# Performance work log

Hardware: AMD Instinct MI355X
Metric: run time of the kernel (lower is better)

Reference implementation:

```python
import jax, jax.numpy as jnp
import numpy as np

M, K, N = 4096, 7168, 18432  # tokens, in_features, out_features


def setup_inputs() -> dict:
    key = jax.random.key(0)
    kx, kw, ks = jax.random.split(key, 3)
    x = jax.random.normal(kx, (M, K), dtype=jnp.float32)
    # int8 quantized weight, layout [in_features, out_features] as in the torch module
    weight = jax.random.randint(kw, (K, N), -128, 128, dtype=jnp.int8)
    # per-output-channel dequant scale (bf16 in the original; fp32 here for a stable baseline)
    scale = jax.random.uniform(ks, (N,), dtype=jnp.float32) * 0.02 + 1e-3
    return {"x": x, "weight": weight, "scale": scale}


def reference(x, weight, scale):
    # Fused dequant + GEMM: y = x @ (int8_weight * scale_per_out_channel)
    w = weight.astype(x.dtype) * scale.astype(x.dtype)[None, :]  # [K, N]
    return x @ w  # [M, N]
```

## Files before the change

kernel.cpp:

```cpp
#include <hip/hip_runtime.h>
#include <hip/hip_bf16.h>
#include <cstdint>
#include <cstddef>

#define M_ 4096
#define K_ 7168
#define N_ 18432

typedef __attribute__((ext_vector_type(4))) int i32x4;

#define AS1 __attribute__((address_space(1)))
#define AS3 __attribute__((address_space(3)))

__device__ __forceinline__ void gld_lds16(void* lds, const void* g) {
  __builtin_amdgcn_global_load_lds((const AS1 void*)g, (AS3 void*)lds, 16, 0, 0);
}

__global__ __launch_bounds__(256) void quant_x_kernel(const float* __restrict__ x,
                                                      signed char* __restrict__ xq,
                                                      float* __restrict__ sx) {
  const int m = blockIdx.x;
  const float4* row4 = (const float4*)(x + (size_t)m * K_);
  float mx = 0.f;
  for (int i = threadIdx.x; i < K_ / 4; i += 256) {
    float4 v = row4[i];
    mx = fmaxf(mx, fmaxf(fmaxf(fabsf(v.x), fabsf(v.y)), fmaxf(fabsf(v.z), fabsf(v.w))));
  }
#pragma unroll
  for (int d = 1; d < 64; d <<= 1) mx = fmaxf(mx, __shfl_xor(mx, d));
  __shared__ float wred[4];
  if ((threadIdx.x & 63) == 0) wred[threadIdx.x >> 6] = mx;
  __syncthreads();
  mx = fmaxf(fmaxf(wred[0], wred[1]), fmaxf(wred[2], wred[3]));
  const float inv = mx > 0.f ? 127.f / mx : 0.f;
  if (threadIdx.x == 0) sx[m] = mx / 127.f;
  char4* q4 = (char4*)(xq + (size_t)m * K_);
  for (int i = threadIdx.x; i < K_ / 4; i += 256) {
    float4 v = row4[i];
    char4 c;
    c.x = (signed char)__float2int_rn(v.x * inv);
    c.y = (signed char)__float2int_rn(v.y * inv);
    c.z = (signed char)__float2int_rn(v.z * inv);
    c.w = (signed char)__float2int_rn(v.w * inv);
    q4[i] = c;
  }
}

__global__ __launch_bounds__(256) void transpose_w_kernel(const int* __restrict__ W,
                                                          signed char* __restrict__ Wt) {
  __shared__ __align__(16) signed char t[64][80];
  const int k0 = blockIdx.x * 64;
  const int n0 = blockIdx.y * 64;
  const int r = threadIdx.x >> 4;
  const int c4 = (threadIdx.x & 15) * 4;
#pragma unroll
  for (int rr = 0; rr < 4; ++rr) {
    const int row = rr * 16 + r;
    int4 v = *(const int4*)(W + (size_t)(k0 + row) * N_ + n0 + c4);
    t[c4 + 0][row] = (signed char)v.x;
    t[c4 + 1][row] = (signed char)v.y;
    t[c4 + 2][row] = (signed char)v.z;
    t[c4 + 3][row] = (signed char)v.w;
  }
  __syncthreads();
  const int nr = threadIdx.x >> 2;
  const int cb = (threadIdx.x & 3) * 16;
  int4 o = *(const int4*)&t[nr][cb];
  *(int4*)(Wt + (size_t)(n0 + nr) * K_ + k0 + cb) = o;
}

__global__ __launch_bounds__(256) void gemm_i8_kernel(const signed char* __restrict__ Aq,
                                                      const signed char* __restrict__ Bt,
                                                      const float* __restrict__ sx,
                                                      const float* __restrict__ scale,
                                                      float* __restrict__ C) {
  __shared__ __align__(16) signed char As[8192];
  __shared__ __align__(16) signed char Bs[8192];

  const int NBN = N_ / 128;
  const int per = (M_ / 128) * NBN / 8;
  const int bid = blockIdx.x;
  const int swz = (bid & 7) * per + (bid >> 3);
  const int bm = swz / NBN;
  const int bn = swz % NBN;
  const int m0 = bm * 128;
  const int n0 = bn * 128;

  const int tid = threadIdx.x;
  const int wid = tid >> 6;
  const int lane = tid & 63;
  const int wrow = wid >> 1;
  const int wcol = wid & 1;

  const int sr = tid >> 2;
  const int sc = (tid & 3) << 4;
  const signed char* a_src0 = Aq + (size_t)(m0 + sr) * K_ + sc;
  const signed char* a_src1 = a_src0 + (size_t)64 * K_;
  const signed char* b_src0 = Bt + (size_t)(n0 + sr) * K_ + sc;
  const signed char* b_src1 = b_src0 + (size_t)64 * K_;
  signed char* a_dst0 = As + wid * 1024;
  signed char* a_dst1 = As + 4096 + wid * 1024;
  signed char* b_dst0 = Bs + wid * 1024;
  signed char* b_dst1 = Bs + 4096 + wid * 1024;

  const int fr = lane & 15;
  const int ko = lane >> 4;
  const int a_off = (wrow * 64 + fr) * 64 + ko * 16;
  const int b_off = (wcol * 64 + fr) * 64 + ko * 16;

  i32x4 acc[4][4] = {};

  for (int k = 0; k < K_; k += 64) {
    gld_lds16(a_dst0, a_src0 + k);
    gld_lds16(a_dst1, a_src1 + k);
    gld_lds16(b_dst0, b_src0 + k);
    gld_lds16(b_dst1, b_src1 + k);
    __syncthreads();

    i32x4 av[4], bv[4];
#pragma unroll
    for (int i = 0; i < 4; ++i) av[i] = *(const i32x4*)(As + a_off + i * 1024);
#pragma unroll
    for (int j = 0; j < 4; ++j) bv[j] = *(const i32x4*)(Bs + b_off + j * 1024);
#pragma unroll
    for (int i = 0; i < 4; ++i)
#pragma unroll
      for (int j = 0; j < 4; ++j)
        acc[i][j] = __builtin_amdgcn_mfma_i32_16x16x64_i8(av[i], bv[j], acc[i][j], 0, 0, 0);
    __syncthreads();
  }

  const int mb = m0 + wrow * 64;
  const int nb = n0 + wcol * 64;
  const int col = lane & 15;
  const int rq = (lane >> 4) * 4;
  float scl[4];
#pragma unroll
  for (int j = 0; j < 4; ++j) scl[j] = scale[nb + j * 16 + col];
#pragma unroll
  for (int i = 0; i < 4; ++i) {
#pragma unroll
    for (int r = 0; r < 4; ++r) {
      const int m = mb + i * 16 + rq + r;
      const float s = sx[m];
      float* out = C + (size_t)m * N_ + nb + col;
#pragma unroll
      for (int j = 0; j < 4; ++j) out[j * 16] = (float)acc[i][j][r] * s * scl[j];
    }
  }
}

__global__ __launch_bounds__(256) void fb_gemm_kernel(const float* __restrict__ X,
                                                      const int* __restrict__ W,
                                                      const float* __restrict__ scale,
                                                      float* __restrict__ Y) {
  __shared__ float xs[16][65];
  __shared__ float ws_[16][65];
  const int bn = blockIdx.x * 64;
  const int bm = blockIdx.y * 64;
  const int tx = threadIdx.x & 15;
  const int ty = threadIdx.x >> 4;
  float acc[4][4] = {};
  for (int k0 = 0; k0 < K_; k0 += 16) {
    for (int i = threadIdx.x; i < 64 * 16; i += 256) {
      int r = i >> 4, c = i & 15;
      xs[c][r] = X[(size_t)(bm + r) * K_ + k0 + c];
    }
    for (int i = threadIdx.x; i < 16 * 64; i += 256) {
      int r = i >> 6, c = i & 63;
      ws_[r][c] = (float)W[(size_t)(k0 + r) * N_ + bn + c];
    }
    __syncthreads();
#pragma unroll
    for (int kk = 0; kk < 16; ++kk) {
      float a[4], b[4];
#pragma unroll
      for (int i = 0; i < 4; ++i) a[i] = xs[kk][ty * 4 + i];
#pragma unroll
      for (int j = 0; j < 4; ++j) b[j] = ws_[kk][tx * 4 + j];
#pragma unroll
      for (int i = 0; i < 4; ++i)
#pragma unroll
        for (int j = 0; j < 4; ++j) acc[i][j] += a[i] * b[j];
    }
    __syncthreads();
  }
#pragma unroll
  for (int i = 0; i < 4; ++i)
#pragma unroll
    for (int j = 0; j < 4; ++j)
      Y[(size_t)(bm + ty * 4 + i) * N_ + bn + tx * 4 + j] = acc[i][j] * scale[bn + tx * 4 + j];
}

extern "C" void kernel_launch(void* const* d_in, const int* in_sizes, int n_in,
                              void* d_out, int out_size, void* d_ws, size_t ws_size,
                              hipStream_t stream) {
  const float* x = (const float*)d_in[0];
  const int* w = (const int*)d_in[1];
  const float* scale = (const float*)d_in[2];
  float* y = (float*)d_out;

  const size_t xq_bytes = (size_t)M_ * K_;
  const size_t sx_off = xq_bytes;
  const size_t wt_off = sx_off + (size_t)M_ * 4;
  const size_t need = wt_off + (size_t)N_ * K_;

  if (ws_size >= need) {
    signed char* xq = (signed char*)d_ws;
    float* sx = (float*)((char*)d_ws + sx_off);
    signed char* wt = (signed char*)((char*)d_ws + wt_off);
    hipLaunchKernelGGL(quant_x_kernel, dim3(M_), dim3(256), 0, stream, x, xq, sx);
    hipLaunchKernelGGL(transpose_w_kernel, dim3(K_ / 64, N_ / 64), dim3(256), 0, stream, w, wt);
    hipLaunchKernelGGL(gemm_i8_kernel, dim3((M_ / 128) * (N_ / 128)), dim3(256), 0, stream,
                       xq, wt, sx, scale, y);
  } else {
    hipLaunchKernelGGL(fb_gemm_kernel, dim3(N_ / 64, M_ / 64), dim3(256), 0, stream,
                       x, w, scale, y);
  }
}
```

Before: 896.6 us.

## Rewrite int8 GEMM with 256x256 tiles, double-buffered LDS and swizzled loads

Replaces the 128x128, single-buffered int8 MFMA GEMM with a 256x256 tile run by 512 threads. Each step covers K=128 split into two 64-wide halves, and global-to-LDS prefetch is double-buffered and interleaved with MFMA phases using explicit waitcnt, barriers and setprio. An XOR swizzle on the LDS layout is meant to avoid bank conflicts. The aim is to hide global load latency and raise arithmetic intensity, at the cost of 128KB of LDS per block, heavy register use, and a fragile hand-tuned schedule.

```diff
diff --git a/kernel.cpp b/kernel.cpp
--- a/kernel.cpp
+++ b/kernel.cpp
@@ -6,6 +6,8 @@
 #define M_ 4096
 #define K_ 7168
 #define N_ 18432
+#define NT 56
+#define ITERS 28
 
 typedef __attribute__((ext_vector_type(4))) int i32x4;
 
@@ -69,85 +71,153 @@
   *(int4*)(Wt + (size_t)(n0 + nr) * K_ + k0 + cb) = o;
 }
 
-__global__ __launch_bounds__(256) void gemm_i8_kernel(const signed char* __restrict__ Aq,
-                                                      const signed char* __restrict__ Bt,
-                                                      const float* __restrict__ sx,
-                                                      const float* __restrict__ scale,
-                                                      float* __restrict__ C) {
-  __shared__ __align__(16) signed char As[8192];
-  __shared__ __align__(16) signed char Bs[8192];
-
-  const int NBN = N_ / 128;
-  const int per = (M_ / 128) * NBN / 8;
+__global__ __launch_bounds__(512, 2) void gemm_i8_kernel(const signed char* __restrict__ Aq,
+                                                         const signed char* __restrict__ Bt,
+                                                         const float* __restrict__ sx,
+                                                         const float* __restrict__ scale,
+                                                         float* __restrict__ C) {
+  __shared__ __align__(16) signed char lds[131072];
+
+  const int NBN = 72;
+  const int per = 144;
   const int bid = blockIdx.x;
   const int swz = (bid & 7) * per + (bid >> 3);
-  const int bm = swz / NBN;
-  const int bn = swz % NBN;
-  const int m0 = bm * 128;
-  const int n0 = bn * 128;
+  const int m0 = (swz / NBN) * 256;
+  const int n0 = (swz % NBN) * 256;
 
   const int tid = threadIdx.x;
-  const int wid = tid >> 6;
+  const int w = tid >> 6;
   const int lane = tid & 63;
-  const int wrow = wid >> 1;
-  const int wcol = wid & 1;
-
-  const int sr = tid >> 2;
-  const int sc = (tid & 3) << 4;
-  const signed char* a_src0 = Aq + (size_t)(m0 + sr) * K_ + sc;
-  const signed char* a_src1 = a_src0 + (size_t)64 * K_;
-  const signed char* b_src0 = Bt + (size_t)(n0 + sr) * K_ + sc;
-  const signed char* b_src1 = b_src0 + (size_t)64 * K_;
-  signed char* a_dst0 = As + wid * 1024;
-  signed char* a_dst1 = As + 4096 + wid * 1024;
-  signed char* b_dst0 = Bs + wid * 1024;
-  signed char* b_dst1 = Bs + 4096 + wid * 1024;
+  const int wr = w >> 2;
+  const int wc = w & 3;
 
   const int fr = lane & 15;
-  const int ko = lane >> 4;
-  const int a_off = (wrow * 64 + fr) * 64 + ko * 16;
-  const int b_off = (wcol * 64 + fr) * 64 + ko * 16;
-
-  i32x4 acc[4][4] = {};
-
-  for (int k = 0; k < K_; k += 64) {
-    gld_lds16(a_dst0, a_src0 + k);
-    gld_lds16(a_dst1, a_src1 + k);
-    gld_lds16(b_dst0, b_src0 + k);
-    gld_lds16(b_dst1, b_src1 + k);
-    __syncthreads();
-
-    i32x4 av[4], bv[4];
-#pragma unroll
-    for (int i = 0; i < 4; ++i) av[i] = *(const i32x4*)(As + a_off + i * 1024);
-#pragma unroll
-    for (int j = 0; j < 4; ++j) bv[j] = *(const i32x4*)(Bs + b_off + j * 1024);
-#pragma unroll
-    for (int i = 0; i < 4; ++i)
-#pragma unroll
-      for (int j = 0; j < 4; ++j)
-        acc[i][j] = __builtin_amdgcn_mfma_i32_16x16x64_i8(av[i], bv[j], acc[i][j], 0, 0, 0);
-    __syncthreads();
-  }
-
-  const int mb = m0 + wrow * 64;
-  const int nb = n0 + wcol * 64;
+  const int q = lane >> 4;
+  const int sl = ((q ^ ((fr >> 1) & 3)) << 4);
+
+  const int ls16 = (((lane & 3) ^ ((lane >> 3) & 3)) << 4);
+  const int pr0 = w * 16 + (lane >> 2);
+  const unsigned offA0 = (unsigned)(m0 + pr0) * K_ + ls16;
+  const unsigned offA1 = (unsigned)(m0 + 128 + pr0) * K_ + ls16;
+  const unsigned offB0 = (unsigned)(n0 + pr0) * K_ + ls16;
+  const unsigned offB1 = (unsigned)(n0 + 128 + pr0) * K_ + ls16;
+
+#define STAGE_A(T, KS) do {                                                        \
+    const int tc_ = (T) < NT ? (T) : NT - 1;                                       \
+    signed char* d_ = lds + (((T) & 1) * 32768 + (KS) * 16384 + w * 1024);         \
+    gld_lds16(d_, Aq + (size_t)offA0 + tc_ * 128 + (KS) * 64);                     \
+    gld_lds16(d_ + 8192, Aq + (size_t)offA1 + tc_ * 128 + (KS) * 64);              \
+  } while (0)
+#define STAGE_B(T, KS) do {                                                        \
+    const int tc_ = (T) < NT ? (T) : NT - 1;                                       \
+    signed char* d_ = lds + (65536 + ((T) & 1) * 32768 + (KS) * 16384 + w * 1024); \
+    gld_lds16(d_, Bt + (size_t)offB0 + tc_ * 128 + (KS) * 64);                     \
+    gld_lds16(d_ + 8192, Bt + (size_t)offB1 + tc_ * 128 + (KS) * 64);              \
+  } while (0)
+#define LDA(BUF, KS, MH) do {                                                      \
+    const signed char* ab = lds + ((BUF) * 32768 + (KS) * 16384);                  \
+    _Pragma("unroll") for (int i_ = 0; i_ < 4; ++i_)                               \
+      aq[i_] = *(const i32x4*)(ab + (wr * 128 + ((MH) * 4 + i_) * 16 + fr) * 64 + sl); \
+  } while (0)
+#define LDB(BUF, KS) do {                                                          \
+    const signed char* bb = lds + (65536 + (BUF) * 32768 + (KS) * 16384);          \
+    _Pragma("unroll") for (int n_ = 0; n_ < 4; ++n_)                               \
+      bq[n_] = *(const i32x4*)(bb + (wc * 64 + n_ * 16 + fr) * 64 + sl);           \
+  } while (0)
+#define MFMA16(MH) do {                                                            \
+    __builtin_amdgcn_s_setprio(1);                                                 \
+    _Pragma("unroll") for (int i_ = 0; i_ < 4; ++i_)                               \
+    _Pragma("unroll") for (int n_ = 0; n_ < 4; ++n_)                               \
+      acc[(MH) * 4 + i_][n_] = __builtin_amdgcn_mfma_i32_16x16x64_i8(              \
+          aq[i_], bq[n_], acc[(MH) * 4 + i_][n_], 0, 0, 0);                        \
+    __builtin_amdgcn_s_setprio(0);                                                 \
+  } while (0)
+#define FENCE asm volatile("" ::: "memory")
+#define BAR do { FENCE; __builtin_amdgcn_s_barrier(); FENCE; } while (0)
+#define LGKM0 asm volatile("s_waitcnt lgkmcnt(0)")
+#define VM6 asm volatile("s_waitcnt vmcnt(6)")
+
+  i32x4 acc[8][4] = {};
+  i32x4 aq[4], bq[4];
+
+  STAGE_B(0, 0); STAGE_A(0, 0); STAGE_B(0, 1); STAGE_A(0, 1);
+  STAGE_B(1, 0); STAGE_A(1, 0); STAGE_B(1, 1);
+  VM6;
+  BAR;
+
+  for (int it = 0; it < ITERS; ++it) {
+    const int u = 2 * it;
+    LDB(0, 0); LDA(0, 0, 0);
+    STAGE_A(u + 1, 1);
+    BAR; LGKM0;
+    MFMA16(0);
+    BAR;
+    LDA(0, 0, 1);
+    STAGE_B(u + 2, 0);
+    BAR; LGKM0;
+    MFMA16(1);
+    BAR;
+    LDB(0, 1); LDA(0, 1, 0);
+    STAGE_A(u + 2, 0);
+    BAR; LGKM0;
+    MFMA16(0);
+    BAR;
+    LDA(0, 1, 1);
+    STAGE_B(u + 2, 1);
+    BAR; LGKM0;
+    MFMA16(1);
+    VM6;
+    BAR;
+    LDB(1, 0); LDA(1, 0, 0);
+    STAGE_A(u + 2, 1);
+    BAR; LGKM0;
+    MFMA16(0);
+    BAR;
+    LDA(1, 0, 1);
+    STAGE_B(u + 3, 0);
+    BAR; LGKM0;
+    MFMA16(1);
+    BAR;
+    LDB(1, 1); LDA(1, 1, 0);
+    STAGE_A(u + 3, 0);
+    BAR; LGKM0;
+    MFMA16(0);
+    BAR;
+    LDA(1, 1, 1);
+    STAGE_B(u + 3, 1);
+    BAR; LGKM0;
+    MFMA16(1);
+    VM6;
+    BAR;
+  }
+
+  const int mb = m0 + wr * 128;
+  const int nb = n0 + wc * 64;
   const int col = lane & 15;
   const int rq = (lane >> 4) * 4;
   float scl[4];
 #pragma unroll
-  for (int j = 0; j < 4; ++j) scl[j] = scale[nb + j * 16 + col];
-#pragma unroll
-  for (int i = 0; i < 4; ++i) {
+  for (int n = 0; n < 4; ++n) scl[n] = scale[nb + n * 16 + col];
+#pragma unroll
+  for (int m = 0; m < 8; ++m) {
 #pragma unroll
     for (int r = 0; r < 4; ++r) {
-      const int m = mb + i * 16 + rq + r;
-      const float s = sx[m];
-      float* out = C + (size_t)m * N_ + nb + col;
-#pragma unroll
-      for (int j = 0; j < 4; ++j) out[j * 16] = (float)acc[i][j][r] * s * scl[j];
-    }
-  }
+      const int row = mb + m * 16 + rq + r;
+      const float s = sx[row];
+      float* out = C + (size_t)row * N_ + nb + col;
+#pragma unroll
+      for (int n = 0; n < 4; ++n) out[n * 16] = (float)acc[m][n][r] * s * scl[n];
+    }
+  }
+#undef STAGE_A
+#undef STAGE_B
+#undef LDA
+#undef LDB
+#undef MFMA16
+#undef FENCE
+#undef BAR
+#undef LGKM0
+#undef VM6
 }
 
 __global__ __launch_bounds__(256) void fb_gemm_kernel(const float* __restrict__ X,
@@ -211,7 +281,7 @@
     signed char* wt = (signed char*)((char*)d_ws + wt_off);
     hipLaunchKernelGGL(quant_x_kernel, dim3(M_), dim3(256), 0, stream, x, xq, sx);
     hipLaunchKernelGGL(transpose_w_kernel, dim3(K_ / 64, N_ / 64), dim3(256), 0, stream, w, wt);
-    hipLaunchKernelGGL(gemm_i8_kernel, dim3((M_ / 128) * (N_ / 128)), dim3(256), 0, stream,
+    hipLaunchKernelGGL(gemm_i8_kernel, dim3((M_ / 256) * (N_ / 256)), dim3(512), 0, stream,
                        xq, wt, sx, scale, y);
   } else {
     hipLaunchKernelGGL(fb_gemm_kernel, dim3(N_ / 64, M_ / 64), dim3(256), 0, stream,
```

After: 723.5 us. 19.3% less time.
